# Performance work log

Hardware: AMD Instinct MI355X
Metric: run time of the kernel (lower is better)

The kernel has to match this reference:

```python
import jax, jax.numpy as jnp
import numpy as np

NUM_HEADS = 32
HEAD_DIM = 128
NUM_KV_HEADS = 8
SCALE = HEAD_DIM ** -0.5
SNAPKV_LIMIT = 512   # context.snapkv_limit
SAMPLE_Q = 128       # context.snapkv_sample_queries default
B = 4                # number of sequences (uniform length)
L = 1024             # tokens per sequence
NUM_SLOTS = 8192
NEG = jnp.float32(-1e30)


def setup_inputs() -> dict:
    key = jax.random.key(0)
    k0, k1, k2 = jax.random.split(key, 3)
    N = B * L
    q = jax.random.normal(k0, (N, NUM_HEADS, HEAD_DIM), jnp.float32)
    k = jax.random.normal(k1, (N, NUM_KV_HEADS, HEAD_DIM), jnp.float32)
    v = jax.random.normal(k2, (N, NUM_KV_HEADS, HEAD_DIM), jnp.float32)
    D = NUM_KV_HEADS * HEAD_DIM
    k_cache = jnp.zeros((NUM_SLOTS, D), jnp.float32)
    v_cache = jnp.zeros((NUM_SLOTS, D), jnp.float32)
    slot_mapping = jnp.arange(N, dtype=jnp.int32)
    cu_seqlens = jnp.arange(B + 1, dtype=jnp.int32) * L
    return dict(q=q, k=k, v=v, k_cache=k_cache, v_cache=v_cache,
                slot_mapping=slot_mapping, cu_seqlens=cu_seqlens)


def _forward(q, k, v, k_cache, v_cache, slot_mapping, cu_seqlens):
    N, H, Dh = q.shape
    Hkv = k.shape[1]
    rep = H // Hkv
    nb = cu_seqlens.shape[0] - 1
    Ls = N // nb  # uniform seq length
    qb = q.reshape(nb, Ls, H, Dh)
    kb = k.reshape(nb, Ls, Hkv, Dh)
    vb = v.reshape(nb, Ls, Hkv, Dh)

    # ---- SnapKV selection (per sequence, vectorized over batch) ----
    q_s = qb[:, Ls - SAMPLE_Q:]                       # [B, SQ, H, Dh] last queries
    k_rep = jnp.repeat(kb, rep, axis=2)               # GQA expand -> [B, L, H, Dh]
    logits = jnp.einsum('bqhd,bkhd->bhqk', q_s, k_rep) * SCALE
    abs_q = jnp.arange(Ls - SAMPLE_Q, Ls)
    abs_k = jnp.arange(Ls)
    allowed = abs_k[None, :] <= abs_q[:, None]        # [SQ, L] causal for sampled q
    logits = jnp.where(allowed[None, None], logits, NEG)
    attn = jax.nn.softmax(logits, axis=-1)
    importance = attn.sum(axis=(1, 2))                # [B, L] sum over heads+queries
    _, idx = jax.lax.top_k(importance, SNAPKV_LIMIT)
    keep_idx = jnp.sort(idx, axis=-1)                 # [B, limit] sorted kept positions

    # ---- compact KV-cache store (store_kvcache on kept tokens) ----
    kept_k = jnp.take_along_axis(kb, keep_idx[:, :, None, None], axis=1)  # [B,limit,Hkv,Dh]
    kept_v = jnp.take_along_axis(vb, keep_idx[:, :, None, None], axis=1)
    # compact slots: first num_kept (= limit) slots of each sequence
    slots = slot_mapping.reshape(nb, Ls)[:, :SNAPKV_LIMIT].reshape(-1)
    D = Hkv * Dh
    k_cache_new = k_cache.at[slots].set(kept_k.reshape(-1, D))
    v_cache_new = v_cache.at[slots].set(kept_v.reshape(-1, D))

    # ---- prefill attention (flash_attn_varlen_func, causal, raw k/v) ----
    v_rep = jnp.repeat(vb, rep, axis=2)               # [B, L, H, Dh]
    scores = jnp.einsum('bqhd,bkhd->bhqk', qb, k_rep) * SCALE
    causal = abs_k[None, :] <= abs_k[:, None]         # [L, L]
    scores = jnp.where(causal[None, None], scores, NEG)
    p = jax.nn.softmax(scores, axis=-1)
    o = jnp.einsum('bhqk,bkhd->bqhd', p, v_rep).reshape(N, H, Dh)
    return o, k_cache_new, v_cache_new


def reference(q, k, v, k_cache, v_cache, slot_mapping, cu_seqlens):
    return _forward(q, k, v, k_cache, v_cache, slot_mapping, cu_seqlens)
```

## Files before the change

### kernel.cpp

```cpp
#include <hip/hip_runtime.h>

#define B_ 4
#define L_ 1024
#define H_ 32
#define HKV_ 8
#define DH_ 128
#define SCALE_ 0.08838834764831845f
#define M_FIX 20.0f
#define KEEP_ 512
#define O_ELEMS (B_*L_*H_*DH_)
#define CACHE_ELEMS (8192*HKV_*DH_)
#define TILE_US 8192
#define QTAB_US 2097152

typedef short short8 __attribute__((ext_vector_type(8)));
typedef float floatx4 __attribute__((ext_vector_type(4)));
typedef unsigned int uintx2 __attribute__((ext_vector_type(2)));
typedef unsigned int uintx4 __attribute__((ext_vector_type(4)));

__device__ inline unsigned short bf16r(float x) {
    unsigned int u = __builtin_bit_cast(unsigned int, x);
    u += 0x7fffu + ((u >> 16) & 1u);
    return (unsigned short)(u >> 16);
}
__device__ inline unsigned int pk_bf16(float a, float b) {
    return (unsigned int)bf16r(a) | ((unsigned int)bf16r(b) << 16);
}
__device__ inline float bf16tof(unsigned short h) {
    unsigned int u = ((unsigned int)h) << 16;
    return __builtin_bit_cast(float, u);
}

__global__ __launch_bounds__(256)
void convert_kernel(const float* __restrict__ Kp, const float* __restrict__ Vp,
                    const float* __restrict__ Qp,
                    unsigned short* __restrict__ Kb, unsigned short* __restrict__ Klo,
                    unsigned short* __restrict__ VTb,
                    unsigned short* __restrict__ Qh, unsigned short* __restrict__ Ql)
{
    int bid = blockIdx.x;
    int kt = bid & 15, hkv = (bid >> 4) & 7, b = bid >> 7;
    int t = threadIdx.x;
    size_t tile = (size_t)bid * TILE_US;

    #pragma unroll
    for (int i = 0; i < 4; ++i) {
        int pos = t + 256 * i;
        int col = pos >> 4, gd = pos & 15;
        const float* kb = &Kp[((size_t)(b * L_ + kt * 64 + col) * HKV_ + hkv) * DH_ + gd * 8];
        float x[8];
        *(float4*)&x[0] = *(const float4*)kb;
        *(float4*)&x[4] = *(const float4*)(kb + 4);
        unsigned int gh[4], gl[4];
        #pragma unroll
        for (int j = 0; j < 4; ++j) {
            unsigned short h0 = bf16r(x[2*j]),   h1 = bf16r(x[2*j+1]);
            unsigned short l0 = bf16r(x[2*j]   - bf16tof(h0));
            unsigned short l1 = bf16r(x[2*j+1] - bf16tof(h1));
            gh[j] = (unsigned int)h0 | ((unsigned int)h1 << 16);
            gl[j] = (unsigned int)l0 | ((unsigned int)l1 << 16);
        }
        int phys = gd ^ (col & 15);
        *(uintx4*)&Kb[tile + col * 128 + phys * 8]  = (uintx4){gh[0], gh[1], gh[2], gh[3]};
        *(uintx4*)&Klo[tile + col * 128 + phys * 8] = (uintx4){gl[0], gl[1], gl[2], gl[3]};
    }

    {
        int d4g = t & 31, g = t >> 5;
        const float* vb = &Vp[((size_t)(b * L_ + kt * 64 + g * 8) * HKV_ + hkv) * DH_ + d4g * 4];
        const size_t vs = (size_t)HKV_ * DH_;
        float4 r[8];
        #pragma unroll
        for (int j = 0; j < 8; ++j) r[j] = *(const float4*)(vb + (size_t)j * vs);
        #pragma unroll
        for (int ii = 0; ii < 4; ++ii) {
            int d = d4g * 4 + ii;
            int phys = g ^ (d & 7);
            uintx4 gp;
            gp[0] = pk_bf16(((const float*)&r[0])[ii], ((const float*)&r[1])[ii]);
            gp[1] = pk_bf16(((const float*)&r[2])[ii], ((const float*)&r[3])[ii]);
            gp[2] = pk_bf16(((const float*)&r[4])[ii], ((const float*)&r[5])[ii]);
            gp[3] = pk_bf16(((const float*)&r[6])[ii], ((const float*)&r[7])[ii]);
            *(uintx4*)&VTb[tile + d * 64 + phys * 8] = gp;
        }
    }

    if (bid < 256) {
        int qts = bid & 1;
        int h   = (bid >> 1) & 31;
        int qb_ = bid >> 6;
        int w = t >> 6, l = t & 63, lm = l & 15, hq = l >> 4;
        int q0 = 896 + qts * 64;
        const float* qb = Qp + ((size_t)(qb_ * L_ + q0 + w * 16 + lm) * H_ + h) * DH_;
        #pragma unroll
        for (int c = 0; c < 4; ++c) {
            int dc = hq * 8 + 32 * c;
            float x[8];
            *(float4*)&x[0] = *(const float4*)(qb + dc);
            *(float4*)&x[4] = *(const float4*)(qb + dc + 4);
            short8 fh, fl;
            #pragma unroll
            for (int j = 0; j < 8; ++j) {
                float xs = x[j] * SCALE_;
                unsigned short hb = bf16r(xs);
                fh[j] = (short)hb;
                fl[j] = (short)bf16r(xs - bf16tof(hb));
            }
            size_t idx = (((size_t)bid * 4 + c) * 256 + t) * 8;
            *(short8*)&Qh[idx] = fh;
            *(short8*)&Ql[idx] = fl;
        }
    }
}

__global__ __launch_bounds__(512, 4)
void attn_mfma(const float* __restrict__ Qp, const unsigned short* __restrict__ Kbp,
               const unsigned short* __restrict__ VTp, float* __restrict__ Op)
{
    __shared__ __align__(16) unsigned short k_lds[64 * 128];
    __shared__ __align__(16) unsigned short vT[128 * 64];
    __shared__ __align__(16) unsigned short p_lds[8 * 1024];

    int bid = (blockIdx.x & 7) * 64 + (blockIdx.x >> 3);
    int pr  = bid & 7;
    int hp  = (bid >> 3) & 1;
    int hkv = (bid >> 4) & 7;
    int b   = bid >> 7;
    int t = threadIdx.x;
    int w = t >> 6;
    int l = t & 63;
    int lm = l & 15;
    int hq = l >> 4;
    int h  = hkv * 4 + hp * 2 + (w >> 2);
    int wi = w & 3;

    for (int ph = 0; ph < 2; ++ph) {
        int qt = ph ? (15 - pr) : pr;

        short8 aq[4];
        {
            const float* qb = Qp + ((size_t)(b * L_ + qt * 64 + wi * 16 + lm) * H_ + h) * DH_;
            #pragma unroll
            for (int c = 0; c < 4; ++c) {
                int dc = hq * 8 + 32 * c;
                float4 x0 = *(const float4*)(qb + dc);
                float4 x1 = *(const float4*)(qb + dc + 4);
                uintx4 packed;
                packed[0] = pk_bf16(x0.x * SCALE_, x0.y * SCALE_);
                packed[1] = pk_bf16(x0.z * SCALE_, x0.w * SCALE_);
                packed[2] = pk_bf16(x1.x * SCALE_, x1.y * SCALE_);
                packed[3] = pk_bf16(x1.z * SCALE_, x1.w * SCALE_);
                aq[c] = __builtin_bit_cast(short8, packed);
            }
        }

        floatx4 O[8];
        #pragma unroll
        for (int n = 0; n < 8; ++n) O[n] = (floatx4){0.f, 0.f, 0.f, 0.f};
        float l_acc[4] = {0.f, 0.f, 0.f, 0.f};

        for (int kt = 0; kt <= qt; ++kt) {
            __syncthreads();
            size_t tbase = (size_t)((b * HKV_ + hkv) * 16 + kt) * TILE_US;
            {
                const uintx4* kg = (const uintx4*)(Kbp + tbase) + t;
                const uintx4* vg = (const uintx4*)(VTp + tbase) + t;
                uintx4* kd = (uintx4*)k_lds + t;
                uintx4* vd = (uintx4*)vT + t;
                #pragma unroll
                for (int i = 0; i < 2; ++i) {
                    kd[i * 512] = kg[i * 512];
                    vd[i * 512] = vg[i * 512];
                }
            }
            __syncthreads();

            floatx4 S[4];
            #pragma unroll
            for (int c = 0; c < 4; ++c) S[c] = (floatx4){-M_FIX, -M_FIX, -M_FIX, -M_FIX};
            #pragma unroll
            for (int kc = 0; kc < 4; ++kc) {
                #pragma unroll
                for (int c = 0; c < 4; ++c) {
                    int row = lm * 4 + c;
                    int phys = (kc * 4 + hq) ^ (row & 15);
                    short8 bk = *(const short8*)&k_lds[row * 128 + phys * 8];
                    S[c] = __builtin_amdgcn_mfma_f32_16x16x32_bf16(aq[kc], bk, S[c], 0, 0, 0);
                }
            }
            bool diag = (kt == qt);
            #pragma unroll
            for (int r = 0; r < 4; ++r) {
                float e0 = __expf(S[0][r]);
                float e1 = __expf(S[1][r]);
                float e2 = __expf(S[2][r]);
                float e3 = __expf(S[3][r]);
                if (diag) {
                    int qabs = qt * 64 + wi * 16 + hq * 4 + r;
                    int kb0 = kt * 64 + lm * 4;
                    e0 = (kb0 + 0 <= qabs) ? e0 : 0.f;
                    e1 = (kb0 + 1 <= qabs) ? e1 : 0.f;
                    e2 = (kb0 + 2 <= qabs) ? e2 : 0.f;
                    e3 = (kb0 + 3 <= qabs) ? e3 : 0.f;
                }
                l_acc[r] += (e0 + e1) + (e2 + e3);
                int m = hq * 4 + r;
                int phys = (lm >> 1) ^ (m & 7);
                uintx2 gp;
                gp[0] = pk_bf16(e0, e1);
                gp[1] = pk_bf16(e2, e3);
                *(uintx2*)&p_lds[w * 1024 + m * 64 + phys * 8 + (lm & 1) * 4] = gp;
            }
            asm volatile("" ::: "memory");
            int phys0 = hq ^ (lm & 7);
            int phys1 = (4 + hq) ^ (lm & 7);
            short8 bp0 = *(const short8*)&p_lds[w * 1024 + lm * 64 + phys0 * 8];
            short8 bp1 = *(const short8*)&p_lds[w * 1024 + lm * 64 + phys1 * 8];
            #pragma unroll
            for (int n = 0; n < 8; ++n) {
                int d = n * 16 + lm;
                short8 a0 = *(const short8*)&vT[d * 64 + (hq ^ (d & 7)) * 8];
                O[n] = __builtin_amdgcn_mfma_f32_16x16x32_bf16(a0, bp0, O[n], 0, 0, 0);
                short8 a1 = *(const short8*)&vT[d * 64 + (((4 + hq) ^ (d & 7))) * 8];
                O[n] = __builtin_amdgcn_mfma_f32_16x16x32_bf16(a1, bp1, O[n], 0, 0, 0);
            }
        }
        #pragma unroll
        for (int r = 0; r < 4; ++r) {
            l_acc[r] += __shfl_xor(l_acc[r], 1);
            l_acc[r] += __shfl_xor(l_acc[r], 2);
            l_acc[r] += __shfl_xor(l_acc[r], 4);
            l_acc[r] += __shfl_xor(l_acc[r], 8);
        }
        float* lf = (float*)&p_lds[w * 1024];
        if (lm == 0) {
            #pragma unroll
            for (int r = 0; r < 4; ++r) lf[hq * 4 + r] = l_acc[r];
        }
        asm volatile("" ::: "memory");
        __builtin_amdgcn_wave_barrier();
        float invl = 1.0f / lf[lm];
        #pragma unroll
        for (int n = 0; n < 8; ++n) {
            float4 res;
            res.x = O[n][0] * invl; res.y = O[n][1] * invl;
            res.z = O[n][2] * invl; res.w = O[n][3] * invl;
            *(float4*)&Op[((size_t)(b * L_ + qt * 64 + wi * 16 + lm) * H_ + h) * DH_ + n * 16 + hq * 4] = res;
        }
    }
}

__global__ __launch_bounds__(256)
void imp_lsum_kernel(const unsigned short* __restrict__ Qhp, const unsigned short* __restrict__ Qlp,
                     const unsigned short* __restrict__ Kbp, const unsigned short* __restrict__ Klop,
                     float* __restrict__ lpart, float* __restrict__ imp)
{
    __shared__ __align__(16) unsigned short khi[64 * 128];
    __shared__ __align__(16) unsigned short klo[64 * 128];

    int bid = blockIdx.x;
    int chunk = bid & 3;
    int qts = (bid >> 2) & 1;
    int h   = (bid >> 3) & 31;
    int b   = bid >> 8;
    int hkv = h >> 2;
    int qblock = (b * 32 + h) * 2 + qts;
    int t = threadIdx.x;
    int w = t >> 6;
    int l = t & 63;
    int lm = l & 15;
    int hq = l >> 4;
    int q0 = 896 + qts * 64;
    int ktd = q0 >> 6;
    int kt_lo = chunk * 4;
    int kt_hi = min(kt_lo + 3, ktd);

    if (bid < 16) imp[bid * 256 + t] = 0.f;

    short8 aqh[4], aql[4];
    #pragma unroll
    for (int c = 0; c < 4; ++c) {
        size_t idx = (((size_t)qblock * 4 + c) * 256 + t) * 8;
        aqh[c] = *(const short8*)&Qhp[idx];
        aql[c] = *(const short8*)&Qlp[idx];
    }

    float l_acc[4] = {0.f, 0.f, 0.f, 0.f};
    for (int kt = kt_lo; kt <= kt_hi; ++kt) {
        __syncthreads();
        size_t tbase = (size_t)((b * HKV_ + hkv) * 16 + kt) * TILE_US;
        {
            const uintx4* hg = (const uintx4*)(Kbp + tbase) + t;
            const uintx4* lg = (const uintx4*)(Klop + tbase) + t;
            uintx4* hd = (uintx4*)khi + t;
            uintx4* ld = (uintx4*)klo + t;
            #pragma unroll
            for (int i = 0; i < 4; ++i) {
                hd[i * 256] = hg[i * 256];
                ld[i * 256] = lg[i * 256];
            }
        }
        __syncthreads();

        floatx4 S[4];
        #pragma unroll
        for (int c = 0; c < 4; ++c) S[c] = (floatx4){-M_FIX, -M_FIX, -M_FIX, -M_FIX};
        #pragma unroll
        for (int kc = 0; kc < 4; ++kc) {
            #pragma unroll
            for (int c = 0; c < 4; ++c) {
                int row = lm * 4 + c;
                int phys = (kc * 4 + hq) ^ (row & 15);
                short8 bh = *(const short8*)&khi[row * 128 + phys * 8];
                short8 bl = *(const short8*)&klo[row * 128 + phys * 8];
                S[c] = __builtin_amdgcn_mfma_f32_16x16x32_bf16(aqh[kc], bh, S[c], 0, 0, 0);
                S[c] = __builtin_amdgcn_mfma_f32_16x16x32_bf16(aqh[kc], bl, S[c], 0, 0, 0);
                S[c] = __builtin_amdgcn_mfma_f32_16x16x32_bf16(aql[kc], bh, S[c], 0, 0, 0);
            }
        }
        bool diag = (kt == ktd);
        #pragma unroll
        for (int r = 0; r < 4; ++r) {
            int qabs = q0 + w * 16 + hq * 4 + r;
            #pragma unroll
            for (int c = 0; c < 4; ++c) {
                float ev = __expf(S[c][r]);
                if (diag) {
                    int kabs = kt * 64 + lm * 4 + c;
                    ev = (kabs <= qabs) ? ev : 0.f;
                }
                l_acc[r] += ev;
            }
        }
    }
    #pragma unroll
    for (int r = 0; r < 4; ++r) {
        l_acc[r] += __shfl_xor(l_acc[r], 1);
        l_acc[r] += __shfl_xor(l_acc[r], 2);
        l_acc[r] += __shfl_xor(l_acc[r], 4);
        l_acc[r] += __shfl_xor(l_acc[r], 8);
    }
    if (lm == 0) {
        #pragma unroll
        for (int r = 0; r < 4; ++r) {
            int row = w * 16 + hq * 4 + r;
            lpart[((size_t)qblock * 64 + row) * 4 + chunk] = l_acc[r];
        }
    }
}

__global__ __launch_bounds__(256, 4)
void imp_col_kernel(const unsigned short* __restrict__ Qhp, const unsigned short* __restrict__ Qlp,
                    const unsigned short* __restrict__ Kbp, const unsigned short* __restrict__ Klop,
                    const float* __restrict__ lpart, float* __restrict__ imp)
{
    __shared__ __align__(16) unsigned short khi[64 * 128];
    __shared__ __align__(16) unsigned short klo[64 * 128];
    __shared__ float imp_loc[64];

    int bid = (blockIdx.x & 7) * 256 + (blockIdx.x >> 3);
    int kt = bid & 15;
    int h  = (bid >> 4) & 31;
    int b  = bid >> 9;
    int hkv = h >> 2;
    int t = threadIdx.x;
    int w = t >> 6;
    int l = t & 63;
    int lm = l & 15;
    int hq = l >> 4;

    if (t < 64) imp_loc[t] = 0.f;
    size_t tbase = (size_t)((b * HKV_ + hkv) * 16 + kt) * TILE_US;
    {
        const uintx4* hg = (const uintx4*)(Kbp + tbase) + t;
        const uintx4* lg = (const uintx4*)(Klop + tbase) + t;
        uintx4* hd = (uintx4*)khi + t;
        uintx4* ld = (uintx4*)klo + t;
        #pragma unroll
        for (int i = 0; i < 4; ++i) {
            hd[i * 256] = hg[i * 256];
            ld[i * 256] = lg[i * 256];
        }
    }
    __syncthreads();

    float cs[4] = {0.f, 0.f, 0.f, 0.f};
    for (int qp2 = 0; qp2 < 2; ++qp2) {
        if (kt == 15 && qp2 == 0) continue;
        int qbid = (b * 32 + h) * 2 + qp2;
        int q0 = 896 + qp2 * 64;
        short8 aqh[4], aql[4];
        #pragma unroll
        for (int c = 0; c < 4; ++c) {
            size_t idx = (((size_t)qbid * 4 + c) * 256 + t) * 8;
            aqh[c] = *(const short8*)&Qhp[idx];
            aql[c] = *(const short8*)&Qlp[idx];
        }
        floatx4 iv4;
        #pragma unroll
        for (int r = 0; r < 4; ++r) {
            int row = w * 16 + hq * 4 + r;
            float4 p = *(const float4*)&lpart[((size_t)qbid * 64 + row) * 4];
            iv4[r] = 1.0f / ((p.x + p.y) + (p.z + p.w));
        }

        floatx4 S[4];
        #pragma unroll
        for (int c = 0; c < 4; ++c) S[c] = (floatx4){-M_FIX, -M_FIX, -M_FIX, -M_FIX};
        #pragma unroll
        for (int kc = 0; kc < 4; ++kc) {
            #pragma unroll
            for (int c = 0; c < 4; ++c) {
                int row = lm * 4 + c;
                int phys = (kc * 4 + hq) ^ (row & 15);
                short8 bh = *(const short8*)&khi[row * 128 + phys * 8];
                short8 bl = *(const short8*)&klo[row * 128 + phys * 8];
                S[c] = __builtin_amdgcn_mfma_f32_16x16x32_bf16(aqh[kc], bh, S[c], 0, 0, 0);
                S[c] = __builtin_amdgcn_mfma_f32_16x16x32_bf16(aqh[kc], bl, S[c], 0, 0, 0);
                S[c] = __builtin_amdgcn_mfma_f32_16x16x32_bf16(aql[kc], bh, S[c], 0, 0, 0);
            }
        }
        #pragma unroll
        for (int c = 0; c < 4; ++c) {
            int kabs = kt * 64 + lm * 4 + c;
            #pragma unroll
            for (int r = 0; r < 4; ++r) {
                int qabs = q0 + w * 16 + hq * 4 + r;
                float ev = (kabs <= qabs) ? __expf(S[c][r]) : 0.f;
                cs[c] += ev * iv4[r];
            }
        }
    }
    #pragma unroll
    for (int c = 0; c < 4; ++c) {
        cs[c] += __shfl_xor(cs[c], 16);
        cs[c] += __shfl_xor(cs[c], 32);
    }
    if (l < 16) {
        #pragma unroll
        for (int c = 0; c < 4; ++c) atomicAdd(&imp_loc[lm * 4 + c], cs[c]);
    }
    __syncthreads();
    if (t < 64) atomicAdd(&imp[b * L_ + kt * 64 + t], imp_loc[t]);
}

__global__ __launch_bounds__(1024)
void topk_kernel(const float* __restrict__ imp, const int* __restrict__ slot_mapping,
                 int* __restrict__ keep, int* __restrict__ inv)
{
    __shared__ __align__(16) float vals[1024];
    __shared__ int wsum[16];
    int b = blockIdx.x;
    int t = threadIdx.x;
    int lane = t & 63, w = t >> 6;

    if (inv) {
        if (t < 512) inv[b * 1024 + 512 + t] = -1;
        inv[4096 + b * 1024 + t] = -1;
    }

    float vi = imp[b * L_ + t];
    vals[t] = vi;
    __syncthreads();

    int rank = 0;
    for (int jc = 0; jc < 256; ++jc) {
        float4 vv = *(const float4*)&vals[jc * 4];
        int j0 = jc * 4;
        rank += (vv.x > vi || (vv.x == vi && (j0 + 0) < t)) ? 1 : 0;
        rank += (vv.y > vi || (vv.y == vi && (j0 + 1) < t)) ? 1 : 0;
        rank += (vv.z > vi || (vv.z == vi && (j0 + 2) < t)) ? 1 : 0;
        rank += (vv.w > vi || (vv.w == vi && (j0 + 3) < t)) ? 1 : 0;
    }
    int flag = (rank < KEEP_) ? 1 : 0;

    int x = flag;
    #pragma unroll
    for (int d = 1; d < 64; d <<= 1) {
        int n = __shfl_up(x, d);
        if (lane >= d) x += n;
    }
    if (lane == 63) wsum[w] = x;
    __syncthreads();
    int woff = 0;
    for (int ww = 0; ww < w; ++ww) woff += wsum[ww];
    int pos = woff + x - flag;

    if (flag) {
        keep[b * KEEP_ + pos] = t;
        if (inv) {
            int dest = slot_mapping[b * L_ + pos];
            inv[dest] = b * L_ + t;
        }
    }
}

__global__ __launch_bounds__(256)
void cache_out_kernel(const float* __restrict__ kin, const float* __restrict__ vin,
                      const float* __restrict__ kc_in, const float* __restrict__ vc_in,
                      const int* __restrict__ inv,
                      float* __restrict__ kc_out, float* __restrict__ vc_out)
{
    int bid = blockIdx.x;
    int t = threadIdx.x;
    #pragma unroll
    for (int i = 0; i < 4; ++i) {
        int s = bid * 4 + i;
        int src = inv[s];
        const float4* kp = (src >= 0) ? (const float4*)&kin[(size_t)src * 1024]
                                      : (const float4*)&kc_in[(size_t)s * 1024];
        const float4* vp = (src >= 0) ? (const float4*)&vin[(size_t)src * 1024]
                                      : (const float4*)&vc_in[(size_t)s * 1024];
        ((float4*)&kc_out[(size_t)s * 1024])[t] = kp[t];
        ((float4*)&vc_out[(size_t)s * 1024])[t] = vp[t];
    }
}

__global__ __launch_bounds__(256)
void cache_copy_kernel(const float* __restrict__ kc_in, const float* __restrict__ vc_in,
                       float* __restrict__ kc_out, float* __restrict__ vc_out)
{
    size_t idx = (size_t)blockIdx.x * 256 + threadIdx.x;
    const float4* ki = (const float4*)kc_in;
    const float4* vi = (const float4*)vc_in;
    float4* ko = (float4*)kc_out;
    float4* vo = (float4*)vc_out;
    #pragma unroll
    for (int i = 0; i < 4; ++i) {
        size_t off = idx + (size_t)i * 524288;
        ko[off] = ki[off];
        vo[off] = vi[off];
    }
}

__global__ void scatter_kernel(const float* __restrict__ kin, const float* __restrict__ vin,
                               const int* __restrict__ keep, const int* __restrict__ slot_mapping,
                               float* __restrict__ kc_out, float* __restrict__ vc_out)
{
    int bid = blockIdx.x;
    int b = bid >> 9, j = bid & 511;
    int src = b * L_ + keep[b * KEEP_ + j];
    int dst = slot_mapping[b * L_ + j];
    int t = threadIdx.x;
    float4 kv = *(const float4*)&kin[(size_t)src * 1024 + t * 4];
    *(float4*)&kc_out[(size_t)dst * 1024 + t * 4] = kv;
    float4 vv = *(const float4*)&vin[(size_t)src * 1024 + t * 4];
    *(float4*)&vc_out[(size_t)dst * 1024 + t * 4] = vv;
}

extern "C" void kernel_launch(void* const* d_in, const int* in_sizes, int n_in,
                              void* d_out, int out_size, void* d_ws, size_t ws_size,
                              hipStream_t stream)
{
    const float* q = (const float*)d_in[0];
    const float* k = (const float*)d_in[1];
    const float* v = (const float*)d_in[2];
    const float* k_cache = (const float*)d_in[3];
    const float* v_cache = (const float*)d_in[4];
    const int* slot_mapping = (const int*)d_in[5];

    float* o = (float*)d_out;
    float* kc_out = o + O_ELEMS;
    float* vc_out = kc_out + CACHE_ELEMS;

    float* imp  = (float*)d_ws;
    int*   keep = (int*)(imp + B_ * L_);
    float* invL = (float*)(keep + B_ * KEEP_);
    int*   inv  = (int*)(invL + B_ * H_ * 128);
    bool use_inv = ws_size >= (size_t)(120 * 1024);
    if (!use_inv) inv = nullptr;

    float* lpart = kc_out;

    const size_t SCRATCH_US = (size_t)3 * 512 * TILE_US + (size_t)2 * QTAB_US;
    bool ws_fits = ws_size >= (size_t)(128 * 1024) + SCRATCH_US * sizeof(unsigned short);
    unsigned short* Kb = ws_fits ? (unsigned short*)((char*)d_ws + 128 * 1024)
                                 : (unsigned short*)vc_out;
    unsigned short* Klo = Kb  + (size_t)512 * TILE_US;
    unsigned short* VTb = Klo + (size_t)512 * TILE_US;
    unsigned short* Qh  = VTb + (size_t)512 * TILE_US;
    unsigned short* Ql  = Qh  + (size_t)QTAB_US;

    convert_kernel<<<dim3(512), dim3(256), 0, stream>>>(k, v, q, Kb, Klo, VTb, Qh, Ql);
    attn_mfma<<<dim3(512), dim3(512), 0, stream>>>(q, Kb, VTb, o);
    imp_lsum_kernel<<<dim3(1024), dim3(256), 0, stream>>>(Qh, Ql, Kb, Klo, lpart, imp);
    imp_col_kernel<<<dim3(2048), dim3(256), 0, stream>>>(Qh, Ql, Kb, Klo, lpart, imp);
    topk_kernel<<<dim3(4), dim3(1024), 0, stream>>>(imp, slot_mapping, keep, inv);

    if (use_inv) {
        cache_out_kernel<<<dim3(2048), dim3(256), 0, stream>>>(k, v, k_cache, v_cache, inv, kc_out, vc_out);
    } else {
        cache_copy_kernel<<<dim3(2048), dim3(256), 0, stream>>>(k_cache, v_cache, kc_out, vc_out);
        scatter_kernel<<<dim3(2048), dim3(256), 0, stream>>>(k, v, keep, slot_mapping, kc_out, vc_out);
    }
}
```

Before: 391.4 us.

## Double-buffer K/V tiles in LDS with register prefetch in attention kernel

The attention kernel now keeps two LDS buffers for K and V tiles. It loads the next tile into registers before computing on the current one, then writes it to the other buffer, so there is one barrier per tile instead of two. The aim is to hide global memory latency behind MFMA compute. In exchange LDS use doubles and the launch-bounds occupancy hint drops from 4 to 2 blocks per CU, which may reduce latency hiding from concurrent blocks.

```diff
diff --git a/kernel.cpp b/kernel.cpp
--- a/kernel.cpp
+++ b/kernel.cpp
@@ -113,12 +113,12 @@
     }
 }
 
-__global__ __launch_bounds__(512, 4)
+__global__ __launch_bounds__(512, 2)
 void attn_mfma(const float* __restrict__ Qp, const unsigned short* __restrict__ Kbp,
                const unsigned short* __restrict__ VTp, float* __restrict__ Op)
 {
-    __shared__ __align__(16) unsigned short k_lds[64 * 128];
-    __shared__ __align__(16) unsigned short vT[128 * 64];
+    __shared__ __align__(16) unsigned short k_lds[2][64 * 128];
+    __shared__ __align__(16) unsigned short vT[2][128 * 64];
     __shared__ __align__(16) unsigned short p_lds[8 * 1024];
 
     int bid = (blockIdx.x & 7) * 64 + (blockIdx.x >> 3);
@@ -133,6 +133,7 @@
     int hq = l >> 4;
     int h  = hkv * 4 + hp * 2 + (w >> 2);
     int wi = w & 3;
+    size_t tabbase = (size_t)((b * HKV_ + hkv) * 16) * TILE_US;
 
     for (int ph = 0; ph < 2; ++ph) {
         int qt = ph ? (15 - pr) : pr;
@@ -154,26 +155,34 @@
             }
         }
 
+        {
+            const uintx4* kg = (const uintx4*)(Kbp + tabbase) + t;
+            const uintx4* vg = (const uintx4*)(VTp + tabbase) + t;
+            uintx4* kd = (uintx4*)k_lds[0] + t;
+            uintx4* vd = (uintx4*)vT[0] + t;
+            #pragma unroll
+            for (int i = 0; i < 2; ++i) { kd[i * 512] = kg[i * 512]; vd[i * 512] = vg[i * 512]; }
+        }
+        __syncthreads();
+
         floatx4 O[8];
         #pragma unroll
         for (int n = 0; n < 8; ++n) O[n] = (floatx4){0.f, 0.f, 0.f, 0.f};
         float l_acc[4] = {0.f, 0.f, 0.f, 0.f};
 
+        int cur = 0;
         for (int kt = 0; kt <= qt; ++kt) {
-            __syncthreads();
-            size_t tbase = (size_t)((b * HKV_ + hkv) * 16 + kt) * TILE_US;
-            {
-                const uintx4* kg = (const uintx4*)(Kbp + tbase) + t;
-                const uintx4* vg = (const uintx4*)(VTp + tbase) + t;
-                uintx4* kd = (uintx4*)k_lds + t;
-                uintx4* vd = (uintx4*)vT + t;
+            uintx4 kr[2], vr[2];
+            bool pf = (kt < qt);
+            if (pf) {
+                size_t tb = tabbase + (size_t)(kt + 1) * TILE_US;
+                const uintx4* kg = (const uintx4*)(Kbp + tb) + t;
+                const uintx4* vg = (const uintx4*)(VTp + tb) + t;
                 #pragma unroll
-                for (int i = 0; i < 2; ++i) {
-                    kd[i * 512] = kg[i * 512];
-                    vd[i * 512] = vg[i * 512];
-                }
-            }
-            __syncthreads();
+                for (int i = 0; i < 2; ++i) { kr[i] = kg[i * 512]; vr[i] = vg[i * 512]; }
+            }
+            const unsigned short* kbuf = k_lds[cur];
+            const unsigned short* vbuf = vT[cur];
 
             floatx4 S[4];
             #pragma unroll
@@ -184,7 +193,7 @@
                 for (int c = 0; c < 4; ++c) {
                     int row = lm * 4 + c;
                     int phys = (kc * 4 + hq) ^ (row & 15);
-                    short8 bk = *(const short8*)&k_lds[row * 128 + phys * 8];
+                    short8 bk = *(const short8*)&kbuf[row * 128 + phys * 8];
                     S[c] = __builtin_amdgcn_mfma_f32_16x16x32_bf16(aq[kc], bk, S[c], 0, 0, 0);
                 }
             }
@@ -219,11 +228,20 @@
             #pragma unroll
             for (int n = 0; n < 8; ++n) {
                 int d = n * 16 + lm;
-                short8 a0 = *(const short8*)&vT[d * 64 + (hq ^ (d & 7)) * 8];
+                short8 a0 = *(const short8*)&vbuf[d * 64 + (hq ^ (d & 7)) * 8];
                 O[n] = __builtin_amdgcn_mfma_f32_16x16x32_bf16(a0, bp0, O[n], 0, 0, 0);
-                short8 a1 = *(const short8*)&vT[d * 64 + (((4 + hq) ^ (d & 7))) * 8];
+                short8 a1 = *(const short8*)&vbuf[d * 64 + (((4 + hq) ^ (d & 7))) * 8];
                 O[n] = __builtin_amdgcn_mfma_f32_16x16x32_bf16(a1, bp1, O[n], 0, 0, 0);
             }
+
+            if (pf) {
+                uintx4* kd = (uintx4*)k_lds[cur ^ 1] + t;
+                uintx4* vd = (uintx4*)vT[cur ^ 1] + t;
+                #pragma unroll
+                for (int i = 0; i < 2; ++i) { kd[i * 512] = kr[i]; vd[i * 512] = vr[i]; }
+            }
+            __syncthreads();
+            cur ^= 1;
         }
         #pragma unroll
         for (int r = 0; r < 4; ++r) {
```

Result: slower. 401.8 us (+2.6%).
